# Kernel optimization log

Measured on AMD Instinct MI355X. Metric: run time of the kernel, lower is better.

The kernel has to match this reference:

```python
import jax, jax.numpy as jnp
import numpy as np

PROP_TIME = 1  # matches cspn = Affinity_Propagate(prop_time=1)
# torch ZeroPad2d (left,right,top,bottom) rewritten as ((top,bottom),(left,right)) per gate 1..8
PADS = [((0, 2), (0, 2)), ((0, 2), (1, 1)), ((0, 2), (2, 0)),
        ((1, 1), (0, 2)), ((1, 1), (2, 0)),
        ((2, 0), (0, 2)), ((2, 0), (1, 1)), ((2, 0), (2, 0))]


def _pad8(x):
    # x: (B, C, H, W) -> (B, 8, C, H+2, W+2): the 8 shifted/zero-padded neighbor maps
    return jnp.stack([jnp.pad(x, ((0, 0), (0, 0), pt, pl)) for pt, pl in PADS], axis=1)


def _affinity_norm(g):
    # g: (B, 8, H, W) -> gate_wb (B, 8, H+2, W+2), gate_sum (B, H, W)
    gate_wb = jnp.stack([jnp.pad(g[:, k], ((0, 0), pt, pl))
                         for k, (pt, pl) in enumerate(PADS)], axis=1)
    abs_w = jnp.sum(jnp.abs(gate_wb), axis=1, keepdims=True)  # sum_conv(|gate_wb|)
    gate_wb = gate_wb / abs_w
    gate_sum = jnp.sum(gate_wb, axis=1)[:, 1:-1, 1:-1]
    return gate_wb, gate_sum


def _prop_once(gate_wb, gate_sum, blur):
    # blur: (B, C, H, W); gate_wb broadcasts over channel dim C
    nws = jnp.sum(gate_wb[:, :, None] * _pad8(blur), axis=1)[:, :, 1:-1, 1:-1]
    return (1.0 - gate_sum[:, None]) * blur + nws  # '8sum' norm


def setup_inputs() -> dict:
    key = jax.random.key(0)
    k1, k2 = jax.random.split(key)
    guidance = jax.random.normal(k1, (24, 128, 128, 16), dtype=jnp.float32)
    blur = jax.random.normal(k2, (20, 128, 128, 16), dtype=jnp.float32)
    return {"guidance": guidance, "blur": blur}


def reference(guidance, blur):
    # guidance: (24, H, W, Z); blur: (C, H, W, Z)
    gwx, gsx = _affinity_norm(jnp.transpose(guidance[0:8], (3, 0, 1, 2)))    # (Z,8,H,W)
    gwy, gsy = _affinity_norm(jnp.transpose(guidance[8:16], (2, 0, 1, 3)))   # (W,8,H,Z)
    gwz, gsz = _affinity_norm(jnp.transpose(guidance[16:24], (1, 0, 2, 3)))  # (H,8,W,Z)
    result = blur
    for _ in range(PROP_TIME):
        result = jnp.transpose(_prop_once(gwx, gsx, jnp.transpose(result, (3, 0, 1, 2))), (1, 2, 3, 0))
        result = jnp.transpose(_prop_once(gwy, gsy, jnp.transpose(result, (2, 0, 1, 3))), (1, 2, 0, 3))
        result = jnp.transpose(_prop_once(gwz, gsz, jnp.transpose(result, (1, 0, 2, 3))), (1, 0, 2, 3))
    return result
```

## Files before the change

kernel.cpp:

```cpp
#include <hip/hip_runtime.h>

#define H 128
#define W 128
#define Zd 16
#define C 20
#define HWZ (H * W * Zd)

#define CG 5
#define CPG (C / CG)
#define POSBLOCKS 256
#define NXCD 8
#define CPGF 5

typedef float f4 __attribute__((ext_vector_type(4)));

__device__ __forceinline__ f4 load4(const float* p) { return *(const f4*)p; }
__device__ __forceinline__ f4 load4u(const float* p) {
    f4 r;
    __builtin_memcpy(&r, p, 16);
    return r;
}

__device__ __forceinline__ float dpp_prev(float x) {
    int r = __builtin_amdgcn_update_dpp(0, __builtin_bit_cast(int, x), 0x111, 0xF, 0xF, false);
    return __builtin_bit_cast(float, r);
}
__device__ __forceinline__ float dpp_next(float x) {
    int r = __builtin_amdgcn_update_dpp(0, __builtin_bit_cast(int, x), 0x101, 0xF, 0xF, false);
    return __builtin_bit_cast(float, r);
}

__device__ __forceinline__ void decode(int bid, int tidx, int& cg, int& tid) {
    int xcd = bid & (NXCD - 1);
    int i = bid >> 3;
    cg = i >> 5;
    int pb = (xcd << 5) + (i & 31);
    tid = pb * 256 + tidx;
}

__global__ __launch_bounds__(256) void prop_x(const float* __restrict__ gd,
                                              const float* __restrict__ in,
                                              float* __restrict__ out) {
    int cg, tid;
    decode(blockIdx.x, threadIdx.x, cg, tid);
    const int z4 = (tid & 3) << 2;
    const int w = (tid >> 2) & (W - 1);
    const int h = tid >> 9;

    const int DI[8] = {1, 1, 1, 0, 0, -1, -1, -1};
    const int DJ[8] = {1, 0, -1, 1, -1, 1, 0, -1};

    f4 g[8];
    int noff[8];
    f4 A = {0, 0, 0, 0}, S = {0, 0, 0, 0};
#pragma unroll
    for (int k = 0; k < 8; ++k) {
        int hh = h + DI[k], ww = w + DJ[k];
        bool valid = ((unsigned)hh < H) && ((unsigned)ww < W);
        f4 val = {0, 0, 0, 0};
        if (valid) val = load4(gd + ((k * H + hh) * W + ww) * Zd + z4);
        g[k] = val;
        noff[k] = valid ? (DI[k] * W + DJ[k]) * Zd : 0;
#pragma unroll
        for (int e = 0; e < 4; ++e) A[e] += __builtin_fabsf(val[e]);
        S += val;
    }
    f4 invA = 1.0f / A;
    f4 c0 = 1.0f - S * invA;
#pragma unroll
    for (int k = 0; k < 8; ++k) g[k] *= invA;

    const int base = (h * W + w) * Zd + z4;
#pragma unroll
    for (int cc = 0; cc < CPG; ++cc) {
        const int c = cg * CPG + cc;
        const float* pc = in + c * HWZ + base;
        f4 acc = c0 * load4(pc);
#pragma unroll
        for (int k = 0; k < 8; ++k) acc += g[k] * load4(pc + noff[k]);
        *(f4*)(out + c * HWZ + base) = acc;
    }
}

__global__ __launch_bounds__(512) void prop_yz(const float* __restrict__ gd,
                                               const float* __restrict__ in,
                                               float* __restrict__ out) {
    const int bid = blockIdx.x;
    const int xcd = bid & (NXCD - 1);
    const int i = bid >> 3;
    const int cgf = i >> 4;
    const int h = (xcd << 4) + (i & 15);

    const int t = threadIdx.x;
    const int z4 = (t & 3) << 2;
    const int w = t >> 2;

    __shared__ float yout[CPGF][W][Zd];

    const int DI[8] = {1, 1, 1, 0, 0, -1, -1, -1};
    const int DJ[8] = {1, 0, -1, 1, -1, 1, 0, -1};
    const int base = (h * W + w) * Zd + z4;

    {
        const int gbase = (((8 * H) + h) * W + w) * Zd + z4;
        f4 g[8];
        f4 A = {0, 0, 0, 0}, S = {0, 0, 0, 0};
#pragma unroll
        for (int k = 0; k < 8; ++k) {
            int di = DI[k], dj = DJ[k];
            bool rv = (unsigned)(h + di) < H;
            f4 va = {0, 0, 0, 0};
            if (rv) va = load4(gd + gbase + k * HWZ + di * (W * Zd));
            f4 val;
            if (dj == 0) {
                val = va;
            } else if (dj == -1) {
                val = (f4){dpp_prev(va[3]), va[0], va[1], va[2]};
                if (z4 == 0) val[0] = 0.f;
            } else {
                val = (f4){va[1], va[2], va[3], dpp_next(va[0])};
                if (z4 == 12) val[3] = 0.f;
            }
            g[k] = val;
#pragma unroll
            for (int e = 0; e < 4; ++e) A[e] += __builtin_fabsf(val[e]);
            S += val;
        }
        f4 invA = 1.0f / A;
        f4 c0 = 1.0f - S * invA;
#pragma unroll
        for (int k = 0; k < 8; ++k) g[k] *= invA;

        f4 gp[3] = {g[0], g[3], g[5]};
        f4 gc[3] = {g[1], c0, g[6]};
        f4 gm[3] = {g[2], g[4], g[7]};
        const int DIr[3] = {1, 0, -1};
        int rowoff[3];
#pragma unroll
        for (int r = 0; r < 3; ++r)
            rowoff[r] = ((unsigned)(h + DIr[r]) < H) ? DIr[r] * (W * Zd) : 0;

#pragma unroll
        for (int cc = 0; cc < CPGF; ++cc) {
            const int c = cgf * CPGF + cc;
            const float* pc = in + c * HWZ + base;
            f4 acc = {0, 0, 0, 0};
#pragma unroll
            for (int r = 0; r < 3; ++r) {
                f4 v = load4(pc + rowoff[r]);
                float lo = dpp_prev(v[3]);
                float hi = dpp_next(v[0]);
                acc += gm[r] * (f4){lo, v[0], v[1], v[2]} + gc[r] * v +
                       gp[r] * (f4){v[1], v[2], v[3], hi};
            }
            *(f4*)(&yout[cc][w][z4]) = acc;
        }
    }

    __syncthreads();

    {
        const int gbase = (((16 * H) + h) * W + w) * Zd + z4;
        f4 g[8];
        f4 A = {0, 0, 0, 0}, S = {0, 0, 0, 0};
#pragma unroll
        for (int k = 0; k < 8; ++k) {
            int di = DI[k], dj = DJ[k];
            bool rv = (unsigned)(w + di) < W;
            f4 va = {0, 0, 0, 0};
            if (rv) va = load4(gd + gbase + k * HWZ + di * Zd);
            f4 val;
            if (dj == 0) {
                val = va;
            } else if (dj == -1) {
                val = (f4){dpp_prev(va[3]), va[0], va[1], va[2]};
                if (z4 == 0) val[0] = 0.f;
            } else {
                val = (f4){va[1], va[2], va[3], dpp_next(va[0])};
                if (z4 == 12) val[3] = 0.f;
            }
            g[k] = val;
#pragma unroll
            for (int e = 0; e < 4; ++e) A[e] += __builtin_fabsf(val[e]);
            S += val;
        }
        f4 invA = 1.0f / A;
        f4 c0 = 1.0f - S * invA;
#pragma unroll
        for (int k = 0; k < 8; ++k) g[k] *= invA;

        f4 gp[3] = {g[0], g[3], g[5]};
        f4 gc[3] = {g[1], c0, g[6]};
        f4 gm[3] = {g[2], g[4], g[7]};
        const int DIr[3] = {1, 0, -1};
        int woff[3];
#pragma unroll
        for (int r = 0; r < 3; ++r)
            woff[r] = ((unsigned)(w + DIr[r]) < W) ? DIr[r] * Zd : 0;

#pragma unroll
        for (int cc = 0; cc < CPGF; ++cc) {
            const int c = cgf * CPGF + cc;
            const float* pl = &yout[cc][w][z4];
            f4 acc = {0, 0, 0, 0};
#pragma unroll
            for (int r = 0; r < 3; ++r) {
                f4 v = load4(pl + woff[r]);
                float lo = dpp_prev(v[3]);
                float hi = dpp_next(v[0]);
                acc += gm[r] * (f4){lo, v[0], v[1], v[2]} + gc[r] * v +
                       gp[r] * (f4){v[1], v[2], v[3], hi};
            }
            *(f4*)(out + c * HWZ + base) = acc;
        }
    }
}

extern "C" void kernel_launch(void* const* d_in, const int* in_sizes, int n_in,
                              void* d_out, int out_size, void* d_ws, size_t ws_size,
                              hipStream_t stream) {
    const float* gd = (const float*)d_in[0];
    const float* blur = (const float*)d_in[1];
    float* out = (float*)d_out;
    float* ws = (float*)d_ws;

    prop_x<<<dim3(POSBLOCKS * CG), dim3(256), 0, stream>>>(gd, blur, ws);
    prop_yz<<<dim3(512), dim3(512), 0, stream>>>(gd, ws, out);
}
```

Before: 29.06 us.

## Fuse x-pass and yz-pass into one kernel with a global grid barrier

Merges the two kernel launches into a single persistent kernel of 512 blocks. Each block first computes the x-direction propagation for its row and channel group into the workspace using agent-scope stores, then waits on an atomic counter barrier before running the y and z passes. This removes one kernel launch and its inter-kernel gap. In exchange it adds a memset of the barrier counter, a spin-wait whose cost depends on all blocks being co-resident, and a timeout break that could let blocks read incomplete data.

```diff
diff --git a/kernel.cpp b/kernel.cpp
--- a/kernel.cpp
+++ b/kernel.cpp
@@ -5,21 +5,14 @@
 #define Zd 16
 #define C 20
 #define HWZ (H * W * Zd)
-
-#define CG 5
-#define CPG (C / CG)
-#define POSBLOCKS 256
+#define CHWZ (C * HWZ)
 #define NXCD 8
 #define CPGF 5
+#define NBLOCKS 512
 
 typedef float f4 __attribute__((ext_vector_type(4)));
 
 __device__ __forceinline__ f4 load4(const float* p) { return *(const f4*)p; }
-__device__ __forceinline__ f4 load4u(const float* p) {
-    f4 r;
-    __builtin_memcpy(&r, p, 16);
-    return r;
-}
 
 __device__ __forceinline__ float dpp_prev(float x) {
     int r = __builtin_amdgcn_update_dpp(0, __builtin_bit_cast(int, x), 0x111, 0xF, 0xF, false);
@@ -30,61 +23,18 @@
     return __builtin_bit_cast(float, r);
 }
 
-__device__ __forceinline__ void decode(int bid, int tidx, int& cg, int& tid) {
-    int xcd = bid & (NXCD - 1);
-    int i = bid >> 3;
-    cg = i >> 5;
-    int pb = (xcd << 5) + (i & 31);
-    tid = pb * 256 + tidx;
-}
-
-__global__ __launch_bounds__(256) void prop_x(const float* __restrict__ gd,
-                                              const float* __restrict__ in,
-                                              float* __restrict__ out) {
-    int cg, tid;
-    decode(blockIdx.x, threadIdx.x, cg, tid);
-    const int z4 = (tid & 3) << 2;
-    const int w = (tid >> 2) & (W - 1);
-    const int h = tid >> 9;
-
-    const int DI[8] = {1, 1, 1, 0, 0, -1, -1, -1};
-    const int DJ[8] = {1, 0, -1, 1, -1, 1, 0, -1};
-
-    f4 g[8];
-    int noff[8];
-    f4 A = {0, 0, 0, 0}, S = {0, 0, 0, 0};
-#pragma unroll
-    for (int k = 0; k < 8; ++k) {
-        int hh = h + DI[k], ww = w + DJ[k];
-        bool valid = ((unsigned)hh < H) && ((unsigned)ww < W);
-        f4 val = {0, 0, 0, 0};
-        if (valid) val = load4(gd + ((k * H + hh) * W + ww) * Zd + z4);
-        g[k] = val;
-        noff[k] = valid ? (DI[k] * W + DJ[k]) * Zd : 0;
-#pragma unroll
-        for (int e = 0; e < 4; ++e) A[e] += __builtin_fabsf(val[e]);
-        S += val;
-    }
-    f4 invA = 1.0f / A;
-    f4 c0 = 1.0f - S * invA;
-#pragma unroll
-    for (int k = 0; k < 8; ++k) g[k] *= invA;
-
-    const int base = (h * W + w) * Zd + z4;
-#pragma unroll
-    for (int cc = 0; cc < CPG; ++cc) {
-        const int c = cg * CPG + cc;
-        const float* pc = in + c * HWZ + base;
-        f4 acc = c0 * load4(pc);
-#pragma unroll
-        for (int k = 0; k < 8; ++k) acc += g[k] * load4(pc + noff[k]);
-        *(f4*)(out + c * HWZ + base) = acc;
-    }
-}
-
-__global__ __launch_bounds__(512) void prop_yz(const float* __restrict__ gd,
-                                               const float* __restrict__ in,
-                                               float* __restrict__ out) {
+__device__ __forceinline__ void store4_agent(float* p, f4 v) {
+    union { f4 v; unsigned long long q[2]; } u;
+    u.v = v;
+    __hip_atomic_store((unsigned long long*)p,     u.q[0], __ATOMIC_RELAXED, __HIP_MEMORY_SCOPE_AGENT);
+    __hip_atomic_store((unsigned long long*)p + 1, u.q[1], __ATOMIC_RELAXED, __HIP_MEMORY_SCOPE_AGENT);
+}
+
+__global__ __launch_bounds__(512, 4) void prop_fused(const float* __restrict__ gd,
+                                                     const float* __restrict__ blur,
+                                                     float* __restrict__ ws,
+                                                     float* __restrict__ out,
+                                                     unsigned* __restrict__ bar) {
     const int bid = blockIdx.x;
     const int xcd = bid & (NXCD - 1);
     const int i = bid >> 3;
@@ -100,6 +50,51 @@
     const int DI[8] = {1, 1, 1, 0, 0, -1, -1, -1};
     const int DJ[8] = {1, 0, -1, 1, -1, 1, 0, -1};
     const int base = (h * W + w) * Zd + z4;
+
+    {
+        f4 g[8];
+        int noff[8];
+        f4 A = {0, 0, 0, 0}, S = {0, 0, 0, 0};
+#pragma unroll
+        for (int k = 0; k < 8; ++k) {
+            int hh = h + DI[k], ww = w + DJ[k];
+            bool valid = ((unsigned)hh < H) && ((unsigned)ww < W);
+            f4 val = {0, 0, 0, 0};
+            if (valid) val = load4(gd + ((k * H + hh) * W + ww) * Zd + z4);
+            g[k] = val;
+            noff[k] = valid ? (DI[k] * W + DJ[k]) * Zd : 0;
+#pragma unroll
+            for (int e = 0; e < 4; ++e) A[e] += __builtin_fabsf(val[e]);
+            S += val;
+        }
+        f4 invA = 1.0f / A;
+        f4 c0 = 1.0f - S * invA;
+#pragma unroll
+        for (int k = 0; k < 8; ++k) g[k] *= invA;
+
+#pragma unroll
+        for (int cc = 0; cc < CPGF; ++cc) {
+            const int c = cgf * CPGF + cc;
+            const float* pc = blur + c * HWZ + base;
+            f4 acc = c0 * load4(pc);
+#pragma unroll
+            for (int k = 0; k < 8; ++k) acc += g[k] * load4(pc + noff[k]);
+            store4_agent(ws + c * HWZ + base, acc);
+        }
+    }
+
+    asm volatile("s_waitcnt vmcnt(0)" ::: "memory");
+    __syncthreads();
+    if (t == 0) {
+        __hip_atomic_fetch_add(bar, 1u, __ATOMIC_RELAXED, __HIP_MEMORY_SCOPE_AGENT);
+        int spins = 0;
+        while (__hip_atomic_load(bar, __ATOMIC_RELAXED, __HIP_MEMORY_SCOPE_AGENT) <
+               (unsigned)NBLOCKS) {
+            __builtin_amdgcn_s_sleep(16);
+            if (++spins > (1 << 16)) break;
+        }
+    }
+    __syncthreads();
 
     {
         const int gbase = (((8 * H) + h) * W + w) * Zd + z4;
@@ -143,7 +138,7 @@
 #pragma unroll
         for (int cc = 0; cc < CPGF; ++cc) {
             const int c = cgf * CPGF + cc;
-            const float* pc = in + c * HWZ + base;
+            const float* pc = ws + c * HWZ + base;
             f4 acc = {0, 0, 0, 0};
 #pragma unroll
             for (int r = 0; r < 3; ++r) {
@@ -223,7 +218,8 @@
     const float* blur = (const float*)d_in[1];
     float* out = (float*)d_out;
     float* ws = (float*)d_ws;
-
-    prop_x<<<dim3(POSBLOCKS * CG), dim3(256), 0, stream>>>(gd, blur, ws);
-    prop_yz<<<dim3(512), dim3(512), 0, stream>>>(gd, ws, out);
-}
+    unsigned* bar = (unsigned*)((char*)d_ws + (size_t)CHWZ * 4);
+
+    hipMemsetAsync(bar, 0, 4, stream);
+    prop_fused<<<dim3(NBLOCKS), dim3(512), 0, stream>>>(gd, blur, ws, out, bar);
+}
```

Result: slower. 63.78 us (+119.5%).
